# Optimization experiments

Hardware: AMD Instinct MI355X
Metric: run time of the kernel (lower is better)

Reference implementation:

```python
import jax, jax.numpy as jnp
import numpy as np

B, S, E = 4, 2048, 1024
H, D = 16, 64  # heads, features per head

def setup_inputs() -> dict:
    key = jax.random.key(0)
    ks = jax.random.split(key, 10)
    s_e = 1.0 / np.sqrt(E)
    s_hd = 1.0 / np.sqrt(H * D)
    return {
        "x": jax.random.normal(ks[0], (B, S, E), dtype=jnp.float32),
        "ln_gamma": jnp.ones((E,), jnp.float32),
        "ln_beta": jnp.zeros((E,), jnp.float32),
        "Wq": jax.random.uniform(ks[1], (E, H * D), jnp.float32, -s_e, s_e),
        "bq": jax.random.uniform(ks[2], (H * D,), jnp.float32, -s_e, s_e),
        "Wk": jax.random.uniform(ks[3], (E, H * D), jnp.float32, -s_e, s_e),
        "bk": jax.random.uniform(ks[4], (H * D,), jnp.float32, -s_e, s_e),
        "Wv": jax.random.uniform(ks[5], (E, H * D), jnp.float32, -s_e, s_e),
        "bv": jax.random.uniform(ks[6], (H * D,), jnp.float32, -s_e, s_e),
        "Wo": jax.random.uniform(ks[7], (H * D, E), jnp.float32, -s_hd, s_hd),
        "bo": jax.random.uniform(ks[8], (E,), jnp.float32, -s_hd, s_hd),
    }

def reference(x, ln_gamma, ln_beta, Wq, bq, Wk, bk, Wv, bv, Wo, bo):
    # pre-norm (LayerNorm over last dim, eps=1e-5 as torch default)
    mu = jnp.mean(x, axis=-1, keepdims=True)
    var = jnp.mean(jnp.square(x - mu), axis=-1, keepdims=True)
    xn = (x - mu) / jnp.sqrt(var + 1e-5) * ln_gamma + ln_beta

    q = (xn @ Wq + bq).reshape(B, S, H, D)
    k = (xn @ Wk + bk).reshape(B, S, H, D)
    v = (xn @ Wv + bv).reshape(B, S, H, D)

    score = jnp.einsum('bihd,bjhd->bijh', q, k) / np.sqrt(D).astype(np.float32)
    # causal mask: disallow j > i
    causal = jnp.triu(jnp.ones((S, S), bool), k=1)[None, :, :, None]
    score = jnp.where(causal, -jnp.inf, score)
    probs = jax.nn.softmax(score, axis=2)

    out = jnp.einsum('bijh,bjhd->bihd', probs, v).reshape(B, S, H * D)
    out = out @ Wo + bo
    return out + x
```

## Files before the change

### kernel.cpp

```cpp
#include <hip/hip_runtime.h>
#include <hip/hip_bf16.h>

#define B 4
#define S 2048
#define E 1024
#define H 16
#define D 64
#define M_ROWS (B * S)
#define HD (H * D)
#define QKVW (3 * HD)

#define QBLK 128
#define KVBLK 64

typedef __attribute__((ext_vector_type(8))) short bf16x8;
typedef __attribute__((ext_vector_type(4))) float f32x4;

typedef const __attribute__((address_space(1))) void* gas_ptr;
typedef __attribute__((address_space(3))) void* las_ptr;
#define GLD16(g, l) __builtin_amdgcn_global_load_lds((gas_ptr)(g), (las_ptr)(l), 16, 0, 0)

__global__ void ln_kernel(const float* __restrict__ x,
                          const float* __restrict__ gamma,
                          const float* __restrict__ beta,
                          __hip_bfloat16* __restrict__ xn) {
    const int row = blockIdx.x;
    const float* xr = x + (size_t)row * E;
    __hip_bfloat16* yr = xn + (size_t)row * E;

    float vals[4];
    float sum = 0.f, sumsq = 0.f;
#pragma unroll
    for (int t = 0; t < 4; ++t) {
        float v = xr[threadIdx.x + t * 256];
        vals[t] = v;
        sum += v;
        sumsq += v * v;
    }
#pragma unroll
    for (int o = 32; o > 0; o >>= 1) {
        sum += __shfl_down(sum, o);
        sumsq += __shfl_down(sumsq, o);
    }
    __shared__ float s1[4], s2[4];
    const int wid = threadIdx.x >> 6, lane = threadIdx.x & 63;
    if (lane == 0) { s1[wid] = sum; s2[wid] = sumsq; }
    __syncthreads();
    if (threadIdx.x == 0) {
        float a = s1[0] + s1[1] + s1[2] + s1[3];
        float b2 = s2[0] + s2[1] + s2[2] + s2[3];
        float mu = a / (float)E;
        float var = b2 / (float)E - mu * mu;
        s1[0] = mu;
        s2[0] = rsqrtf(var + 1e-5f);
    }
    __syncthreads();
    const float mu = s1[0], rstd = s2[0];
#pragma unroll
    for (int t = 0; t < 4; ++t) {
        int c = threadIdx.x + t * 256;
        yr[c] = __float2bfloat16((vals[t] - mu) * rstd * gamma[c] + beta[c]);
    }
}

__global__ void transpose_to_bf16(const float* __restrict__ W,
                                  __hip_bfloat16* __restrict__ Wt,
                                  int K, int N) {
    __shared__ float t[64][65];
    const int n0 = blockIdx.x * 64, k0 = blockIdx.y * 64;
    const int tx = threadIdx.x & 63, ty = threadIdx.x >> 6;
#pragma unroll
    for (int i = ty; i < 64; i += 4)
        t[i][tx] = W[(size_t)(k0 + i) * N + n0 + tx];
    __syncthreads();
#pragma unroll
    for (int i = ty; i < 64; i += 4)
        Wt[(size_t)(n0 + i) * K + k0 + tx] = __float2bfloat16(t[tx][i]);
}

__global__ void pack_bias(const float* __restrict__ bq, const float* __restrict__ bk,
                          const float* __restrict__ bv, float* __restrict__ o) {
    const int t = threadIdx.x;
    o[t] = bq[t]; o[HD + t] = bk[t]; o[2 * HD + t] = bv[t];
}

template<bool BF16OUT>
__global__ __launch_bounds__(256)
void gemm_mfma(const __hip_bfloat16* __restrict__ A,
               const __hip_bfloat16* __restrict__ Bt,
               const float* __restrict__ bias,
               const float* __restrict__ residual,
               void* __restrict__ Cout,
               int Mdim, int Ndim, int Kdim) {
    __shared__ __align__(16) short sA[128 * 32];
    __shared__ __align__(16) short sB[128 * 32];

    const int tid = threadIdx.x;
    const int lane = tid & 63;
    const int wv = tid >> 6;
    const int wr = wv >> 1, wc = wv & 1;
    const int fr = lane & 15;
    const int kg = (lane >> 4) * 8;
    const int brow = blockIdx.y * 128;
    const int bcol = blockIdx.x * 128;

    const int r0 = tid >> 2;
    const int sub = (tid & 3) * 8;
    const __hip_bfloat16* gA0 = A + (size_t)(brow + r0) * Kdim + sub;
    const __hip_bfloat16* gA1 = gA0 + (size_t)64 * Kdim;
    const __hip_bfloat16* gB0 = Bt + (size_t)(bcol + r0) * Kdim + sub;
    const __hip_bfloat16* gB1 = gB0 + (size_t)64 * Kdim;

    f32x4 acc[4][4] = {};

    for (int k0 = 0; k0 < Kdim; k0 += 32) {
        GLD16(gA0 + k0, sA + (size_t)tid * 8);
        GLD16(gA1 + k0, sA + (size_t)(256 + tid) * 8);
        GLD16(gB0 + k0, sB + (size_t)tid * 8);
        GLD16(gB1 + k0, sB + (size_t)(256 + tid) * 8);
        __syncthreads();
        bf16x8 af[4], bfr[4];
#pragma unroll
        for (int mi = 0; mi < 4; ++mi)
            af[mi] = *(const bf16x8*)&sA[(wr * 64 + mi * 16 + fr) * 32 + kg];
#pragma unroll
        for (int ni = 0; ni < 4; ++ni)
            bfr[ni] = *(const bf16x8*)&sB[(wc * 64 + ni * 16 + fr) * 32 + kg];
#pragma unroll
        for (int mi = 0; mi < 4; ++mi)
#pragma unroll
            for (int ni = 0; ni < 4; ++ni)
                acc[mi][ni] = __builtin_amdgcn_mfma_f32_16x16x32_bf16(
                    af[mi], bfr[ni], acc[mi][ni], 0, 0, 0);
        __syncthreads();
    }

#pragma unroll
    for (int mi = 0; mi < 4; ++mi) {
        const int rbase = brow + wr * 64 + mi * 16 + ((lane >> 4) << 2);
#pragma unroll
        for (int ni = 0; ni < 4; ++ni) {
            const int c = bcol + wc * 64 + ni * 16 + fr;
            const float bv = bias[c];
#pragma unroll
            for (int qd = 0; qd < 4; ++qd) {
                const size_t idx = (size_t)(rbase + qd) * Ndim + c;
                float v = acc[mi][ni][qd] + bv;
                if constexpr (BF16OUT) {
                    ((__hip_bfloat16*)Cout)[idx] = __float2bfloat16(v);
                } else {
                    ((float*)Cout)[idx] = v + residual[idx];
                }
            }
        }
    }
}

__global__ __launch_bounds__(256)
void flash_attn(const __hip_bfloat16* __restrict__ qkv,
                __hip_bfloat16* __restrict__ og) {
    __shared__ __align__(16) short sK[2][KVBLK * 64];
    __shared__ __align__(16) short sVt[2][64 * KVBLK];
    __shared__ __align__(16) short sP[4][32 * 72];

    const int tid = threadIdx.x;
    const int lane = tid & 63;
    const int wv = tid >> 6;
    const int fr = lane & 15;
    const int g = lane >> 4;

    const int p = blockIdx.x & 7;
    const int bh = blockIdx.x >> 3;
    const int b = bh >> 4, h = bh & 15;

    const __hip_bfloat16* qp = qkv + (size_t)b * S * QKVW + h * D;
    const __hip_bfloat16* kp = qp + HD;
    const unsigned short* vp16 = (const unsigned short*)(qp + 2 * HD);
    const size_t ogBase = (size_t)b * S * HD + h * D;

    const int krow = tid >> 3;
    const int kslot = tid & 7;

#pragma unroll
    for (int qi = 0; qi < 2; ++qi) {
        const int bq = qi ? p : (15 - p);
        const int q0 = bq * QBLK;

        bf16x8 qa[2][2];
#pragma unroll
        for (int mt = 0; mt < 2; ++mt)
#pragma unroll
            for (int c = 0; c < 2; ++c) {
                bf16x8 t = *(const bf16x8*)&qp[(size_t)(q0 + wv * 32 + mt * 16 + fr) * QKVW + c * 32 + g * 8];
                bf16x8 r;
#pragma unroll
                for (int j = 0; j < 8; ++j) {
                    short sb = t[j];
                    __hip_bfloat16 hb = *(__hip_bfloat16*)&sb;
                    float f = __bfloat162float(hb) * 0.125f;
                    __hip_bfloat16 ob = __float2bfloat16(f);
                    r[j] = *(short*)&ob;
                }
                qa[mt][c] = r;
            }

        f32x4 Oacc[2][4] = {};
        float mrun[2] = {-1e30f, -1e30f}, lrun[2] = {0.f, 0.f};

        const int kvmax = 2 * bq + 1;
        const int qmaxw = q0 + wv * 32 + 31;

        __syncthreads();

        bf16x8 kpre[2], vpre[2];
#pragma unroll
        for (int it = 0; it < 2; ++it) {
            kpre[it] = *(const bf16x8*)&kp[(size_t)(krow + it * 32) * QKVW + kslot * 8];
#pragma unroll
            for (int j = 0; j < 8; ++j)
                vpre[it][j] = (short)vp16[(size_t)((wv + it * 4) * 8 + j) * QKVW + lane];
        }

        for (int kvt = 0; kvt <= kvmax; ++kvt) {
            const int kv0 = kvt * KVBLK;
            const int cur = kvt & 1;

#pragma unroll
            for (int it = 0; it < 2; ++it) {
                const int r = krow + it * 32;
                *(bf16x8*)&sK[cur][r * 64 + ((kslot ^ (r & 7)) * 8)] = kpre[it];
                *(bf16x8*)&sVt[cur][lane * 64 + (((wv + it * 4) ^ (lane & 7)) * 8)] = vpre[it];
            }
            __syncthreads();

            if (kvt < kvmax) {
                const int kv0n = kv0 + KVBLK;
#pragma unroll
                for (int it = 0; it < 2; ++it) {
                    kpre[it] = *(const bf16x8*)&kp[(size_t)(kv0n + krow + it * 32) * QKVW + kslot * 8];
#pragma unroll
                    for (int j = 0; j < 8; ++j)
                        vpre[it][j] = (short)vp16[(size_t)(kv0n + (wv + it * 4) * 8 + j) * QKVW + lane];
                }
            }

            if (kv0 <= qmaxw) {
                f32x4 sf[2][4] = {};
#pragma unroll
                for (int nt = 0; nt < 4; ++nt) {
                    const int kr = nt * 16 + fr;
#pragma unroll
                    for (int c = 0; c < 2; ++c) {
                        bf16x8 kb = *(const bf16x8*)&sK[cur][kr * 64 + (((c * 4 + g) ^ (kr & 7)) * 8)];
#pragma unroll
                        for (int mt = 0; mt < 2; ++mt)
                            sf[mt][nt] = __builtin_amdgcn_mfma_f32_16x16x32_bf16(kb, qa[mt][c], sf[mt][nt], 0, 0, 0);
                    }
                }

#pragma unroll
                for (int mt = 0; mt < 2; ++mt) {
                    const int qabs = q0 + wv * 32 + mt * 16 + fr;
                    if (kv0 + KVBLK - 1 > q0 + wv * 32 + mt * 16) {
#pragma unroll
                        for (int nt = 0; nt < 4; ++nt)
#pragma unroll
                            for (int r = 0; r < 4; ++r)
                                if (kv0 + nt * 16 + g * 4 + r > qabs) sf[mt][nt][r] = -1e30f;
                    }
                    float mx = -1e30f;
#pragma unroll
                    for (int nt = 0; nt < 4; ++nt)
#pragma unroll
                        for (int r = 0; r < 4; ++r) mx = fmaxf(mx, sf[mt][nt][r]);
                    mx = fmaxf(mx, __shfl_xor(mx, 16));
                    mx = fmaxf(mx, __shfl_xor(mx, 32));
                    const float mnew = fmaxf(mrun[mt], mx);
                    const float corr = __expf(mrun[mt] - mnew);
                    mrun[mt] = mnew;
                    float rs = 0.f;
#pragma unroll
                    for (int nt = 0; nt < 4; ++nt)
#pragma unroll
                        for (int r = 0; r < 4; ++r) {
                            float pv = __expf(sf[mt][nt][r] - mnew);
                            sf[mt][nt][r] = pv;
                            rs += pv;
                        }
                    rs += __shfl_xor(rs, 16);
                    rs += __shfl_xor(rs, 32);
                    lrun[mt] = lrun[mt] * corr + rs;
#pragma unroll
                    for (int r = 0; r < 4; ++r) {
                        const float corrO = __shfl(corr, g * 4 + r);
#pragma unroll
                        for (int nt = 0; nt < 4; ++nt) Oacc[mt][nt][r] *= corrO;
                    }
#pragma unroll
                    for (int nt = 0; nt < 4; ++nt) {
                        ushort4 pk;
#pragma unroll
                        for (int r = 0; r < 4; ++r) {
                            __hip_bfloat16 pb = __float2bfloat16(sf[mt][nt][r]);
                            ((unsigned short*)&pk)[r] = *(unsigned short*)&pb;
                        }
                        *(ushort4*)&sP[wv][(mt * 16 + fr) * 72 + nt * 16 + g * 4] = pk;
                    }
                }

#pragma unroll
                for (int cp = 0; cp < 2; ++cp) {
                    bf16x8 pa[2];
#pragma unroll
                    for (int mt = 0; mt < 2; ++mt)
                        pa[mt] = *(const bf16x8*)&sP[wv][(mt * 16 + fr) * 72 + cp * 32 + g * 8];
#pragma unroll
                    for (int nt = 0; nt < 4; ++nt) {
                        const int vrow = nt * 16 + fr;
                        bf16x8 vb = *(const bf16x8*)&sVt[cur][vrow * 64 + (((cp * 4 + g) ^ (vrow & 7)) * 8)];
#pragma unroll
                        for (int mt = 0; mt < 2; ++mt)
                            Oacc[mt][nt] = __builtin_amdgcn_mfma_f32_16x16x32_bf16(pa[mt], vb, Oacc[mt][nt], 0, 0, 0);
                    }
                }
            }
        }

#pragma unroll
        for (int mt = 0; mt < 2; ++mt) {
            float rl[4];
#pragma unroll
            for (int r = 0; r < 4; ++r) rl[r] = 1.f / __shfl(lrun[mt], g * 4 + r);
#pragma unroll
            for (int nt = 0; nt < 4; ++nt) {
                const int d = nt * 16 + fr;
#pragma unroll
                for (int r = 0; r < 4; ++r) {
                    const int qrow = q0 + wv * 32 + mt * 16 + g * 4 + r;
                    og[ogBase + (size_t)qrow * HD + d] = __float2bfloat16(Oacc[mt][nt][r] * rl[r]);
                }
            }
        }
    }
}

extern "C" void kernel_launch(void* const* d_in, const int* in_sizes, int n_in,
                              void* d_out, int out_size, void* d_ws, size_t ws_size,
                              hipStream_t stream) {
    const float* x     = (const float*)d_in[0];
    const float* gamma = (const float*)d_in[1];
    const float* beta  = (const float*)d_in[2];
    const float* Wq    = (const float*)d_in[3];
    const float* bq    = (const float*)d_in[4];
    const float* Wk    = (const float*)d_in[5];
    const float* bk    = (const float*)d_in[6];
    const float* Wv    = (const float*)d_in[7];
    const float* bv    = (const float*)d_in[8];
    const float* Wo    = (const float*)d_in[9];
    const float* bo    = (const float*)d_in[10];
    float* out = (float*)d_out;

    const size_t nTok = (size_t)M_ROWS;
    __hip_bfloat16* xn    = (__hip_bfloat16*)d_ws;
    __hip_bfloat16* qkv   = xn + nTok * E;
    __hip_bfloat16* ao    = qkv + nTok * QKVW;
    __hip_bfloat16* Wqkvt = ao + nTok * HD;
    __hip_bfloat16* Wot   = Wqkvt + (size_t)QKVW * E;
    float* bqkv           = (float*)(Wot + (size_t)E * HD);

    dim3 tg(16, 16);
    transpose_to_bf16<<<tg, 256, 0, stream>>>(Wq, Wqkvt,                     E, HD);
    transpose_to_bf16<<<tg, 256, 0, stream>>>(Wk, Wqkvt + (size_t)HD * E,    E, HD);
    transpose_to_bf16<<<tg, 256, 0, stream>>>(Wv, Wqkvt + (size_t)2 * HD * E, E, HD);
    transpose_to_bf16<<<tg, 256, 0, stream>>>(Wo, Wot, HD, E);
    pack_bias<<<1, HD, 0, stream>>>(bq, bk, bv, bqkv);

    ln_kernel<<<M_ROWS, 256, 0, stream>>>(x, gamma, beta, xn);

    dim3 gg(QKVW / 128, M_ROWS / 128);
    gemm_mfma<true><<<gg, 256, 0, stream>>>(xn, Wqkvt, bqkv, nullptr, qkv, M_ROWS, QKVW, E);

    flash_attn<<<dim3(B * H * 8), 256, 0, stream>>>(qkv, ao);

    dim3 go(E / 128, M_ROWS / 128);
    gemm_mfma<false><<<go, 256, 0, stream>>>(ao, Wot, bo, x, (void*)out, M_ROWS, E, HD);
}
```

Baseline: 317.7 us.

## Deepen GEMM K-tile, split attention into one q-block per CTA, lazy rescale

The GEMM now stages a 64-wide K slice per iteration instead of 32, which halves the number of barrier pairs and raises the work done per sync. The flash attention kernel drops the paired q-block loop and launches one CTA per (batch, head, q-block), ordered heaviest first, to raise parallelism. It also folds log2(e) into the Q scale so it can use exp2f. It skips the running-max rescale of the output accumulator when the new max stays within a threshold of the old one. In exchange it gives up the balanced pairing of light and heavy q-blocks, and the GEMM uses more LDS per block.

```diff
diff --git a/kernel.cpp b/kernel.cpp
--- a/kernel.cpp
+++ b/kernel.cpp
@@ -92,8 +92,8 @@
                const float* __restrict__ residual,
                void* __restrict__ Cout,
                int Mdim, int Ndim, int Kdim) {
-    __shared__ __align__(16) short sA[128 * 32];
-    __shared__ __align__(16) short sB[128 * 32];
+    __shared__ __align__(16) short sA[128 * 64];
+    __shared__ __align__(16) short sB[128 * 64];
 
     const int tid = threadIdx.x;
     const int lane = tid & 63;
@@ -104,34 +104,36 @@
     const int brow = blockIdx.y * 128;
     const int bcol = blockIdx.x * 128;
 
-    const int r0 = tid >> 2;
-    const int sub = (tid & 3) * 8;
-    const __hip_bfloat16* gA0 = A + (size_t)(brow + r0) * Kdim + sub;
-    const __hip_bfloat16* gA1 = gA0 + (size_t)64 * Kdim;
-    const __hip_bfloat16* gB0 = Bt + (size_t)(bcol + r0) * Kdim + sub;
-    const __hip_bfloat16* gB1 = gB0 + (size_t)64 * Kdim;
+    const int r0 = tid >> 3;
+    const int slot = tid & 7;
+    const __hip_bfloat16* gA = A + (size_t)(brow + r0) * Kdim + slot * 8;
+    const __hip_bfloat16* gB = Bt + (size_t)(bcol + r0) * Kdim + slot * 8;
 
     f32x4 acc[4][4] = {};
 
-    for (int k0 = 0; k0 < Kdim; k0 += 32) {
-        GLD16(gA0 + k0, sA + (size_t)tid * 8);
-        GLD16(gA1 + k0, sA + (size_t)(256 + tid) * 8);
-        GLD16(gB0 + k0, sB + (size_t)tid * 8);
-        GLD16(gB1 + k0, sB + (size_t)(256 + tid) * 8);
+    for (int k0 = 0; k0 < Kdim; k0 += 64) {
+#pragma unroll
+        for (int i = 0; i < 4; ++i) {
+            GLD16(gA + (size_t)(32 * i) * Kdim + k0, sA + (size_t)(tid + 256 * i) * 8);
+            GLD16(gB + (size_t)(32 * i) * Kdim + k0, sB + (size_t)(tid + 256 * i) * 8);
+        }
         __syncthreads();
-        bf16x8 af[4], bfr[4];
-#pragma unroll
-        for (int mi = 0; mi < 4; ++mi)
-            af[mi] = *(const bf16x8*)&sA[(wr * 64 + mi * 16 + fr) * 32 + kg];
-#pragma unroll
-        for (int ni = 0; ni < 4; ++ni)
-            bfr[ni] = *(const bf16x8*)&sB[(wc * 64 + ni * 16 + fr) * 32 + kg];
-#pragma unroll
-        for (int mi = 0; mi < 4; ++mi)
+#pragma unroll
+        for (int kk = 0; kk < 64; kk += 32) {
+            bf16x8 af[4], bfr[4];
+#pragma unroll
+            for (int mi = 0; mi < 4; ++mi)
+                af[mi] = *(const bf16x8*)&sA[(wr * 64 + mi * 16 + fr) * 64 + kk + kg];
 #pragma unroll
             for (int ni = 0; ni < 4; ++ni)
-                acc[mi][ni] = __builtin_amdgcn_mfma_f32_16x16x32_bf16(
-                    af[mi], bfr[ni], acc[mi][ni], 0, 0, 0);
+                bfr[ni] = *(const bf16x8*)&sB[(wc * 64 + ni * 16 + fr) * 64 + kk + kg];
+#pragma unroll
+            for (int mi = 0; mi < 4; ++mi)
+#pragma unroll
+                for (int ni = 0; ni < 4; ++ni)
+                    acc[mi][ni] = __builtin_amdgcn_mfma_f32_16x16x32_bf16(
+                        af[mi], bfr[ni], acc[mi][ni], 0, 0, 0);
+        }
         __syncthreads();
     }
 
@@ -169,9 +171,10 @@
     const int fr = lane & 15;
     const int g = lane >> 4;
 
-    const int p = blockIdx.x & 7;
-    const int bh = blockIdx.x >> 3;
+    const int bh = blockIdx.x & 63;
+    const int bq = 15 - (int)(blockIdx.x >> 6);
     const int b = bh >> 4, h = bh & 15;
+    const int q0 = bq * QBLK;
 
     const __hip_bfloat16* qp = qkv + (size_t)b * S * QKVW + h * D;
     const __hip_bfloat16* kp = qp + HD;
@@ -181,164 +184,166 @@
     const int krow = tid >> 3;
     const int kslot = tid & 7;
 
-#pragma unroll
-    for (int qi = 0; qi < 2; ++qi) {
-        const int bq = qi ? p : (15 - p);
-        const int q0 = bq * QBLK;
-
-        bf16x8 qa[2][2];
-#pragma unroll
-        for (int mt = 0; mt < 2; ++mt)
-#pragma unroll
-            for (int c = 0; c < 2; ++c) {
-                bf16x8 t = *(const bf16x8*)&qp[(size_t)(q0 + wv * 32 + mt * 16 + fr) * QKVW + c * 32 + g * 8];
-                bf16x8 r;
-#pragma unroll
-                for (int j = 0; j < 8; ++j) {
-                    short sb = t[j];
-                    __hip_bfloat16 hb = *(__hip_bfloat16*)&sb;
-                    float f = __bfloat162float(hb) * 0.125f;
-                    __hip_bfloat16 ob = __float2bfloat16(f);
-                    r[j] = *(short*)&ob;
-                }
-                qa[mt][c] = r;
-            }
-
-        f32x4 Oacc[2][4] = {};
-        float mrun[2] = {-1e30f, -1e30f}, lrun[2] = {0.f, 0.f};
-
-        const int kvmax = 2 * bq + 1;
-        const int qmaxw = q0 + wv * 32 + 31;
-
+    const float qscale = 0.125f * 1.44269504088896f;
+    bf16x8 qa[2][2];
+#pragma unroll
+    for (int mt = 0; mt < 2; ++mt)
+#pragma unroll
+        for (int c = 0; c < 2; ++c) {
+            bf16x8 t = *(const bf16x8*)&qp[(size_t)(q0 + wv * 32 + mt * 16 + fr) * QKVW + c * 32 + g * 8];
+            bf16x8 r;
+#pragma unroll
+            for (int j = 0; j < 8; ++j) {
+                short sb = t[j];
+                __hip_bfloat16 hb = *(__hip_bfloat16*)&sb;
+                float f = __bfloat162float(hb) * qscale;
+                __hip_bfloat16 ob = __float2bfloat16(f);
+                r[j] = *(short*)&ob;
+            }
+            qa[mt][c] = r;
+        }
+
+    f32x4 Oacc[2][4] = {};
+    float mrun[2] = {-1e30f, -1e30f}, lrun[2] = {0.f, 0.f};
+
+    const int kvmax = 2 * bq + 1;
+    const int qmaxw = q0 + wv * 32 + 31;
+
+    bf16x8 kpre[2], vpre[2];
+#pragma unroll
+    for (int it = 0; it < 2; ++it) {
+        kpre[it] = *(const bf16x8*)&kp[(size_t)(krow + it * 32) * QKVW + kslot * 8];
+#pragma unroll
+        for (int j = 0; j < 8; ++j)
+            vpre[it][j] = (short)vp16[(size_t)((wv + it * 4) * 8 + j) * QKVW + lane];
+    }
+
+    for (int kvt = 0; kvt <= kvmax; ++kvt) {
+        const int kv0 = kvt * KVBLK;
+        const int cur = kvt & 1;
+
+#pragma unroll
+        for (int it = 0; it < 2; ++it) {
+            const int r = krow + it * 32;
+            *(bf16x8*)&sK[cur][r * 64 + ((kslot ^ (r & 7)) * 8)] = kpre[it];
+            *(bf16x8*)&sVt[cur][lane * 64 + (((wv + it * 4) ^ (lane & 7)) * 8)] = vpre[it];
+        }
         __syncthreads();
 
-        bf16x8 kpre[2], vpre[2];
-#pragma unroll
-        for (int it = 0; it < 2; ++it) {
-            kpre[it] = *(const bf16x8*)&kp[(size_t)(krow + it * 32) * QKVW + kslot * 8];
-#pragma unroll
-            for (int j = 0; j < 8; ++j)
-                vpre[it][j] = (short)vp16[(size_t)((wv + it * 4) * 8 + j) * QKVW + lane];
-        }
-
-        for (int kvt = 0; kvt <= kvmax; ++kvt) {
-            const int kv0 = kvt * KVBLK;
-            const int cur = kvt & 1;
-
+        if (kvt < kvmax) {
+            const int kv0n = kv0 + KVBLK;
 #pragma unroll
             for (int it = 0; it < 2; ++it) {
-                const int r = krow + it * 32;
-                *(bf16x8*)&sK[cur][r * 64 + ((kslot ^ (r & 7)) * 8)] = kpre[it];
-                *(bf16x8*)&sVt[cur][lane * 64 + (((wv + it * 4) ^ (lane & 7)) * 8)] = vpre[it];
-            }
-            __syncthreads();
-
-            if (kvt < kvmax) {
-                const int kv0n = kv0 + KVBLK;
-#pragma unroll
-                for (int it = 0; it < 2; ++it) {
-                    kpre[it] = *(const bf16x8*)&kp[(size_t)(kv0n + krow + it * 32) * QKVW + kslot * 8];
-#pragma unroll
-                    for (int j = 0; j < 8; ++j)
-                        vpre[it][j] = (short)vp16[(size_t)(kv0n + (wv + it * 4) * 8 + j) * QKVW + lane];
-                }
-            }
-
-            if (kv0 <= qmaxw) {
-                f32x4 sf[2][4] = {};
-#pragma unroll
-                for (int nt = 0; nt < 4; ++nt) {
-                    const int kr = nt * 16 + fr;
-#pragma unroll
-                    for (int c = 0; c < 2; ++c) {
-                        bf16x8 kb = *(const bf16x8*)&sK[cur][kr * 64 + (((c * 4 + g) ^ (kr & 7)) * 8)];
-#pragma unroll
-                        for (int mt = 0; mt < 2; ++mt)
-                            sf[mt][nt] = __builtin_amdgcn_mfma_f32_16x16x32_bf16(kb, qa[mt][c], sf[mt][nt], 0, 0, 0);
+                kpre[it] = *(const bf16x8*)&kp[(size_t)(kv0n + krow + it * 32) * QKVW + kslot * 8];
+#pragma unroll
+                for (int j = 0; j < 8; ++j)
+                    vpre[it][j] = (short)vp16[(size_t)(kv0n + (wv + it * 4) * 8 + j) * QKVW + lane];
+            }
+        }
+
+        if (kv0 <= qmaxw) {
+            f32x4 sf[2][4] = {};
+#pragma unroll
+            for (int nt = 0; nt < 4; ++nt) {
+                const int kr = nt * 16 + fr;
+#pragma unroll
+                for (int c = 0; c < 2; ++c) {
+                    bf16x8 kb = *(const bf16x8*)&sK[cur][kr * 64 + (((c * 4 + g) ^ (kr & 7)) * 8)];
+#pragma unroll
+                    for (int mt = 0; mt < 2; ++mt)
+                        sf[mt][nt] = __builtin_amdgcn_mfma_f32_16x16x32_bf16(kb, qa[mt][c], sf[mt][nt], 0, 0, 0);
+                }
+            }
+
+#pragma unroll
+            for (int mt = 0; mt < 2; ++mt) {
+                const int qabs = q0 + wv * 32 + mt * 16 + fr;
+                if (kv0 + KVBLK - 1 > q0 + wv * 32 + mt * 16) {
+#pragma unroll
+                    for (int nt = 0; nt < 4; ++nt)
+#pragma unroll
+                        for (int r = 0; r < 4; ++r)
+                            if (kv0 + nt * 16 + g * 4 + r > qabs) sf[mt][nt][r] = -1e30f;
+                }
+                float mx = -1e30f;
+#pragma unroll
+                for (int nt = 0; nt < 4; ++nt)
+#pragma unroll
+                    for (int r = 0; r < 4; ++r) mx = fmaxf(mx, sf[mt][nt][r]);
+                mx = fmaxf(mx, __shfl_xor(mx, 16));
+                mx = fmaxf(mx, __shfl_xor(mx, 32));
+
+                const bool nores = __all(mx <= mrun[mt] + 8.f);
+                const float mnew = nores ? mrun[mt] : fmaxf(mrun[mt], mx);
+
+                float rs = 0.f;
+#pragma unroll
+                for (int nt = 0; nt < 4; ++nt)
+#pragma unroll
+                    for (int r = 0; r < 4; ++r) {
+                        float pv = exp2f(sf[mt][nt][r] - mnew);
+                        sf[mt][nt][r] = pv;
+                        rs += pv;
                     }
-                }
-
-#pragma unroll
-                for (int mt = 0; mt < 2; ++mt) {
-                    const int qabs = q0 + wv * 32 + mt * 16 + fr;
-                    if (kv0 + KVBLK - 1 > q0 + wv * 32 + mt * 16) {
-#pragma unroll
-                        for (int nt = 0; nt < 4; ++nt)
-#pragma unroll
-                            for (int r = 0; r < 4; ++r)
-                                if (kv0 + nt * 16 + g * 4 + r > qabs) sf[mt][nt][r] = -1e30f;
-                    }
-                    float mx = -1e30f;
-#pragma unroll
-                    for (int nt = 0; nt < 4; ++nt)
-#pragma unroll
-                        for (int r = 0; r < 4; ++r) mx = fmaxf(mx, sf[mt][nt][r]);
-                    mx = fmaxf(mx, __shfl_xor(mx, 16));
-                    mx = fmaxf(mx, __shfl_xor(mx, 32));
-                    const float mnew = fmaxf(mrun[mt], mx);
-                    const float corr = __expf(mrun[mt] - mnew);
+                rs += __shfl_xor(rs, 16);
+                rs += __shfl_xor(rs, 32);
+
+                if (nores) {
+                    lrun[mt] += rs;
+                } else {
+                    const float corr = exp2f(mrun[mt] - mnew);
+                    lrun[mt] = lrun[mt] * corr + rs;
                     mrun[mt] = mnew;
-                    float rs = 0.f;
-#pragma unroll
-                    for (int nt = 0; nt < 4; ++nt)
-#pragma unroll
-                        for (int r = 0; r < 4; ++r) {
-                            float pv = __expf(sf[mt][nt][r] - mnew);
-                            sf[mt][nt][r] = pv;
-                            rs += pv;
-                        }
-                    rs += __shfl_xor(rs, 16);
-                    rs += __shfl_xor(rs, 32);
-                    lrun[mt] = lrun[mt] * corr + rs;
 #pragma unroll
                     for (int r = 0; r < 4; ++r) {
                         const float corrO = __shfl(corr, g * 4 + r);
 #pragma unroll
                         for (int nt = 0; nt < 4; ++nt) Oacc[mt][nt][r] *= corrO;
                     }
-#pragma unroll
-                    for (int nt = 0; nt < 4; ++nt) {
-                        ushort4 pk;
-#pragma unroll
-                        for (int r = 0; r < 4; ++r) {
-                            __hip_bfloat16 pb = __float2bfloat16(sf[mt][nt][r]);
-                            ((unsigned short*)&pk)[r] = *(unsigned short*)&pb;
-                        }
-                        *(ushort4*)&sP[wv][(mt * 16 + fr) * 72 + nt * 16 + g * 4] = pk;
+                }
+
+#pragma unroll
+                for (int nt = 0; nt < 4; ++nt) {
+                    ushort4 pk;
+#pragma unroll
+                    for (int r = 0; r < 4; ++r) {
+                        __hip_bfloat16 pb = __float2bfloat16(sf[mt][nt][r]);
+                        ((unsigned short*)&pk)[r] = *(unsigned short*)&pb;
                     }
-                }
-
-#pragma unroll
-                for (int cp = 0; cp < 2; ++cp) {
-                    bf16x8 pa[2];
+                    *(ushort4*)&sP[wv][(mt * 16 + fr) * 72 + nt * 16 + g * 4] = pk;
+                }
+            }
+
+#pragma unroll
+            for (int cp = 0; cp < 2; ++cp) {
+                bf16x8 pa[2];
+#pragma unroll
+                for (int mt = 0; mt < 2; ++mt)
+                    pa[mt] = *(const bf16x8*)&sP[wv][(mt * 16 + fr) * 72 + cp * 32 + g * 8];
+#pragma unroll
+                for (int nt = 0; nt < 4; ++nt) {
+                    const int vrow = nt * 16 + fr;
+                    bf16x8 vb = *(const bf16x8*)&sVt[cur][vrow * 64 + (((cp * 4 + g) ^ (vrow & 7)) * 8)];
 #pragma unroll
                     for (int mt = 0; mt < 2; ++mt)
-                        pa[mt] = *(const bf16x8*)&sP[wv][(mt * 16 + fr) * 72 + cp * 32 + g * 8];
-#pragma unroll
-                    for (int nt = 0; nt < 4; ++nt) {
-                        const int vrow = nt * 16 + fr;
-                        bf16x8 vb = *(const bf16x8*)&sVt[cur][vrow * 64 + (((cp * 4 + g) ^ (vrow & 7)) * 8)];
-#pragma unroll
-                        for (int mt = 0; mt < 2; ++mt)
-                            Oacc[mt][nt] = __builtin_amdgcn_mfma_f32_16x16x32_bf16(pa[mt], vb, Oacc[mt][nt], 0, 0, 0);
-                    }
-                }
-            }
-        }
-
-#pragma unroll
-        for (int mt = 0; mt < 2; ++mt) {
-            float rl[4];
-#pragma unroll
-            for (int r = 0; r < 4; ++r) rl[r] = 1.f / __shfl(lrun[mt], g * 4 + r);
-#pragma unroll
-            for (int nt = 0; nt < 4; ++nt) {
-                const int d = nt * 16 + fr;
-#pragma unroll
-                for (int r = 0; r < 4; ++r) {
-                    const int qrow = q0 + wv * 32 + mt * 16 + g * 4 + r;
-                    og[ogBase + (size_t)qrow * HD + d] = __float2bfloat16(Oacc[mt][nt][r] * rl[r]);
-                }
+                        Oacc[mt][nt] = __builtin_amdgcn_mfma_f32_16x16x32_bf16(pa[mt], vb, Oacc[mt][nt], 0, 0, 0);
+                }
+            }
+        }
+    }
+
+#pragma unroll
+    for (int mt = 0; mt < 2; ++mt) {
+        float rl[4];
+#pragma unroll
+        for (int r = 0; r < 4; ++r) rl[r] = 1.f / __shfl(lrun[mt], g * 4 + r);
+#pragma unroll
+        for (int nt = 0; nt < 4; ++nt) {
+            const int d = nt * 16 + fr;
+#pragma unroll
+            for (int r = 0; r < 4; ++r) {
+                const int qrow = q0 + wv * 32 + mt * 16 + g * 4 + r;
+                og[ogBase + (size_t)qrow * HD + d] = __float2bfloat16(Oacc[mt][nt][r] * rl[r]);
             }
         }
     }
@@ -369,8 +374,8 @@
     float* bqkv           = (float*)(Wot + (size_t)E * HD);
 
     dim3 tg(16, 16);
-    transpose_to_bf16<<<tg, 256, 0, stream>>>(Wq, Wqkvt,                     E, HD);
-    transpose_to_bf16<<<tg, 256, 0, stream>>>(Wk, Wqkvt + (size_t)HD * E,    E, HD);
+    transpose_to_bf16<<<tg, 256, 0, stream>>>(Wq, Wqkvt,                      E, HD);
+    transpose_to_bf16<<<tg, 256, 0, stream>>>(Wk, Wqkvt + (size_t)HD * E,     E, HD);
     transpose_to_bf16<<<tg, 256, 0, stream>>>(Wv, Wqkvt + (size_t)2 * HD * E, E, HD);
     transpose_to_bf16<<<tg, 256, 0, stream>>>(Wo, Wot, HD, E);
     pack_bias<<<1, HD, 0, stream>>>(bq, bk, bv, bqkv);
@@ -380,7 +385,7 @@
     dim3 gg(QKVW / 128, M_ROWS / 128);
     gemm_mfma<true><<<gg, 256, 0, stream>>>(xn, Wqkvt, bqkv, nullptr, qkv, M_ROWS, QKVW, E);
 
-    flash_attn<<<dim3(B * H * 8), 256, 0, stream>>>(qkv, ao);
+    flash_attn<<<dim3(B * H * (S / QBLK)), 256, 0, stream>>>(qkv, ao);
 
     dim3 go(E / 128, M_ROWS / 128);
     gemm_mfma<false><<<go, 256, 0, stream>>>(ao, Wot, bo, x, (void*)out, M_ROWS, E, HD);
```

New measurement: 336.2 us. 1.06x slower.
